# Performance work log

Hardware: AMD Instinct MI355X
Metric: run time of the kernel (lower is better)

## Reference

```python
import jax, jax.numpy as jnp
import numpy as np

NUM_BITS = 8
VMIN, VMAX = 0.0, 1.0
THRESH = 4.0
K_SYN = 32


def gray_code_encode(x):
    # (batch, features) -> (batch, features*NUM_BITS) binary float bits
    norm = (jnp.clip(x, VMIN, VMAX) - VMIN) / (VMAX - VMIN)
    levels = jnp.round(norm * (2 ** NUM_BITS - 1)).astype(jnp.int32)
    gray = levels ^ (levels >> 1)
    bit_pos = jnp.arange(NUM_BITS, dtype=jnp.int32)
    bits = ((gray[..., None] >> bit_pos) & 1).astype(jnp.float32)
    return bits.reshape(x.shape[0], -1)


def _make_sparse_weight(key, n_neurons, prev_size):
    # k random synapses per neuron with +/-1 weights (rest zero), as in
    # _initialise_layer_weights (standard, non-dynamic path)
    kc, ks = jax.random.split(key)
    cols = jax.random.randint(kc, (n_neurons, K_SYN), 0, prev_size)
    signs = jax.random.randint(ks, (n_neurons, K_SYN), 0, 2).astype(jnp.float32) * 2 - 1
    rows = jnp.broadcast_to(jnp.arange(n_neurons)[:, None], (n_neurons, K_SYN))
    return jnp.zeros((n_neurons, prev_size), jnp.float32).at[rows, cols].set(signs)


def setup_inputs() -> dict:
    key = jax.random.key(0)
    kx, k0, k1, k2, ko = jax.random.split(key, 5)
    batch, feat = 512, 256
    hidden, classes, n_hidden_layers = 4096, 1000, 3
    enc = feat * NUM_BITS  # 2048
    x = jax.random.uniform(kx, (batch, feat), dtype=jnp.float32)
    W0 = _make_sparse_weight(k0, hidden, enc)
    W1 = _make_sparse_weight(k1, hidden, hidden)
    W2 = _make_sparse_weight(k2, hidden, hidden)
    out_w = jax.random.normal(ko, (n_hidden_layers, hidden, classes), dtype=jnp.float32) * 0.01
    return {"x": x, "W0": W0, "W1": W1, "W2": W2, "out_w": out_w}


def reference(x, W0, W1, W2, out_w):
    prev = gray_code_encode(x)  # (b, enc)
    out = jnp.zeros((x.shape[0], out_w.shape[-1]), jnp.float32)
    for i, W in enumerate((W0, W1, W2)):
        z = prev @ W.T                                  # (b, hidden)
        prev = (z >= THRESH).astype(jnp.float32)        # binary activation
        out = out + prev @ out_w[i]                     # accumulate per-layer
    return out
```

## Files before the change

### kernel.cpp

```cpp
#include <hip/hip_runtime.h>
#include <stdint.h>

typedef unsigned long long u64;
typedef __attribute__((ext_vector_type(8))) short bf16x8;
typedef __attribute__((ext_vector_type(4))) float f32x4;
typedef __attribute__((ext_vector_type(4))) unsigned u32x4;

#define BATCH 512
#define FEAT 256
#define ENC 2048
#define HID 4096
#define CLS 1000
#define KTOT 12288
#define NSPLIT 16
#define KSPLIT 768
#define PARTLD 1024

#define OFF_ENC2   0
#define OFF_ACT2   131072
#define OFF_TABLE  917504
#define OFF_SGN    1703936
#define OFF_WT     2097152
#define OFF_PART   27262976
#define PART_BYTES (16ull * 512 * 1024 * 4)
#define WS_NEED    (OFF_PART + PART_BYTES)

static __device__ inline unsigned short f2bf(float f) {
    unsigned u = __float_as_uint(f);
    return (unsigned short)((u + 0x7FFFu + ((u >> 16) & 1u)) >> 16);
}

static __device__ inline void gld16(const void* g, void* s) {
    __builtin_amdgcn_global_load_lds((const __attribute__((address_space(1))) void*)g,
                                     (__attribute__((address_space(3))) void*)s, 16, 0, 0);
}

__global__ void __launch_bounds__(256)
k_prep(const float* __restrict__ x, u64* __restrict__ enc2,
       const float* __restrict__ W0, const float* __restrict__ W1,
       const float* __restrict__ W2,
       uint16_t* __restrict__ table, char* __restrict__ sgn,
       const float* __restrict__ out_w, short* __restrict__ wt) {
    __shared__ short tile[64 * 68];
    __shared__ int cnt4[4];
    int bid = blockIdx.x;
    int t = threadIdx.x;
    int lane = t & 63;
    int wv = t >> 6;

    if (bid < 512) {
        int wid = bid * 4 + wv;
        int f = wid >> 3, bg = wid & 7;
        float v = x[(size_t)(bg * 64 + lane) * FEAT + f];
        v = fminf(fmaxf(v, 0.0f), 1.0f);
        int lev = (int)rintf(v * 255.0f);
        unsigned gray = (unsigned)(lev ^ (lev >> 1));
        u64 w = 0;
        #pragma unroll
        for (int bit = 0; bit < 8; ++bit) {
            u64 m = __ballot((gray >> bit) & 1u);
            if (lane == bit) w = m;
        }
        if (lane < 8) enc2[(size_t)bg * ENC + f * 8 + lane] = w;
        return;
    }
    if (bid < 5632) {
        int wsid = (bid - 512) * 4 + wv;
        int row, base, cidx;
        if (wsid < HID) { row = wsid; base = 0; cidx = wv; }
        else {
            int w2 = wsid - HID;
            row = HID + (w2 >> 1);
            base = (w2 & 1) * 2048;
            cidx = wv >> 1;
        }
        uint16_t* te = table + (size_t)row * 32;
        char*     se = sgn + (size_t)row * 32;
        if (lane < 8) ((u64*)te)[lane] = 0;
        if (lane < 4) ((u64*)se)[lane] = 0;
        if (t < 4) cnt4[t] = 0;
        __syncthreads();
        const float* Wr;
        if (row < HID)          Wr = W0 + (size_t)row * ENC;
        else if (row < 2 * HID) Wr = W1 + (size_t)(row - HID) * HID + base;
        else                    Wr = W2 + (size_t)(row - 2 * HID) * HID + base;
        const u32x4* p4 = (const u32x4*)Wr;
        u32x4 v[8];
        #pragma unroll
        for (int j = 0; j < 8; ++j) v[j] = __builtin_nontemporal_load(p4 + j * 64 + lane);
        #pragma unroll
        for (int j = 0; j < 8; ++j) {
            unsigned a0 = v[j].x, a1 = v[j].y, a2 = v[j].z, a3 = v[j].w;
            if (a0 | a1 | a2 | a3) {
                int col0 = base + j * 256 + lane * 4;
                if (a0) { int s = atomicAdd(&cnt4[cidx], 1);
                          te[s] = (uint16_t)col0;       se[s] = (a0 >> 31) ? -1 : 1; }
                if (a1) { int s = atomicAdd(&cnt4[cidx], 1);
                          te[s] = (uint16_t)(col0 + 1); se[s] = (a1 >> 31) ? -1 : 1; }
                if (a2) { int s = atomicAdd(&cnt4[cidx], 1);
                          te[s] = (uint16_t)(col0 + 2); se[s] = (a2 >> 31) ? -1 : 1; }
                if (a3) { int s = atomicAdd(&cnt4[cidx], 1);
                          te[s] = (uint16_t)(col0 + 3); se[s] = (a3 >> 31) ? -1 : 1; }
            }
        }
        return;
    }
    {
        int b2 = bid - 5632;
        int kt = b2 % 192, ct = b2 / 192;
        int k0 = kt * 64, c0 = ct * 64;
        {
            int rrow = t >> 4, c4 = t & 15;
            int c = c0 + c4 * 4;
            #pragma unroll
            for (int rd = 0; rd < 4; ++rd) {
                int kl = rd * 16 + rrow;
                f32x4 vv;
                if (c < CLS)
                    vv = __builtin_nontemporal_load(
                        (const f32x4*)&out_w[(size_t)(k0 + kl) * CLS + c]);
                else { vv.x = 0.0f; vv.y = 0.0f; vv.z = 0.0f; vv.w = 0.0f; }
                short* d = &tile[kl * 68 + c4 * 4];
                d[0] = (short)f2bf(vv.x); d[1] = (short)f2bf(vv.y);
                d[2] = (short)f2bf(vv.z); d[3] = (short)f2bf(vv.w);
            }
        }
        __syncthreads();
        {
            int chunk = t & 7, cl2 = t >> 3;
            #pragma unroll
            for (int rd = 0; rd < 2; ++rd) {
                int c_local = rd * 32 + cl2;
                int c = c0 + c_local;
                unsigned s8[8];
                #pragma unroll
                for (int j = 0; j < 8; ++j)
                    s8[j] = (unsigned)(unsigned short)tile[(chunk * 8 + j) * 68 + c_local];
                uint4 pk;
                pk.x = s8[0] | (s8[1] << 16);
                pk.y = s8[2] | (s8[3] << 16);
                pk.z = s8[4] | (s8[5] << 16);
                pk.w = s8[6] | (s8[7] << 16);
                *(uint4*)&wt[(size_t)c * KTOT + k0 + ((chunk ^ (c & 7)) * 8)] = pk;
            }
        }
    }
}

__global__ void __launch_bounds__(256)
k_layer(const u64* __restrict__ prev2, int Kwords,
        const uint16_t* __restrict__ table_l, const char* __restrict__ sgn_l,
        u64* __restrict__ actout) {
    int wid = __builtin_amdgcn_readfirstlane(blockIdx.x * 4 + (threadIdx.x >> 6));
    int lane = threadIdx.x & 63;
    int n = wid >> 3, bg = wid & 7;
    const u64* prow = prev2 + (size_t)bg * Kwords;
    const uint4* tq = (const uint4*)(table_l + (size_t)n * 32);
    const int*  sq = (const int*)(sgn_l + (size_t)n * 32);
    int z = 0;
    #pragma unroll
    for (int q = 0; q < 4; ++q) {
        uint4 e4 = tq[q];
        int s0 = sq[q * 2], s1 = sq[q * 2 + 1];
        unsigned es[4] = {e4.x, e4.y, e4.z, e4.w};
        u64 w[8];
        #pragma unroll
        for (int h = 0; h < 4; ++h) {
            w[h * 2]     = prow[es[h] & 0xFFFFu];
            w[h * 2 + 1] = prow[es[h] >> 16];
        }
        #pragma unroll
        for (int j = 0; j < 8; ++j) {
            int bit = (int)((w[j] >> lane) & 1ull);
            int sw = (j < 4) ? s0 : s1;
            int s = (sw << (24 - (j & 3) * 8)) >> 24;
            z += s * bit;
        }
    }
    u64 res = __ballot(z >= 4);
    if (lane == 0) actout[(size_t)bg * HID + n] = res;
}

template<int MODE>
__global__ void __launch_bounds__(256)
k_gemm(const u64* __restrict__ act2, const short* __restrict__ wt,
       float* __restrict__ out, float* __restrict__ part) {
    __shared__ __attribute__((aligned(16))) short As[128 * 64];
    __shared__ __attribute__((aligned(16))) short Bs[128 * 64];
    int bid = blockIdx.x;
    int mt = bid & 3, nt = (bid >> 2) & 7, ks = bid >> 5;
    int tid = threadIdx.x, lane = tid & 63;
    int wv = tid >> 6, waveM = wv & 1, waveN = wv >> 1;
    int quad = lane >> 4, cl = lane & 15;
    f32x4 acc[4][4] = {};
    const char* Bb = (const char*)(wt + (size_t)nt * 128 * KTOT + ks * KSPLIT);
    int r = tid >> 3, sub = tid & 7;
    for (int kk = 0; kk < KSPLIT; kk += 64) {
        #pragma unroll
        for (int rd = 0; rd < 4; ++rd) {
            size_t go = (size_t)(r + rd * 32) * (KTOT * 2) + kk * 2 + sub * 16;
            gld16(Bb + go, &Bs[(tid + rd * 256) * 8]);
        }
        {
            int kabs = ks * KSPLIT + kk;
            int l = kabs >> 12, nk = kabs & 4095;
            #pragma unroll
            for (int i = 0; i < 4; ++i) {
                int item = i * 256 + tid;
                int rr = item >> 3, gg = item & 7;
                const u64* w8 = act2 + ((size_t)(l * 8 + mt * 2 + (rr >> 6))) * HID + nk + gg * 8;
                int bl = rr & 63;
                unsigned sh[8];
                #pragma unroll
                for (int j = 0; j < 8; ++j)
                    sh[j] = (unsigned)((w8[j] >> bl) & 1ull) * 0x3F80u;
                uint4 pk;
                pk.x = sh[0] | (sh[1] << 16);
                pk.y = sh[2] | (sh[3] << 16);
                pk.z = sh[4] | (sh[5] << 16);
                pk.w = sh[6] | (sh[7] << 16);
                *(uint4*)&As[rr * 64 + ((gg ^ (rr & 7)) * 8)] = pk;
            }
        }
        __syncthreads();
        #pragma unroll
        for (int s = 0; s < 2; ++s) {
            int xr = ((s * 4 + quad) ^ (cl & 7)) * 8;
            bf16x8 af[4], bfr[4];
            #pragma unroll
            for (int mf = 0; mf < 4; ++mf)
                af[mf] = *(const bf16x8*)&As[(waveM * 64 + mf * 16 + cl) * 64 + xr];
            #pragma unroll
            for (int nf = 0; nf < 4; ++nf)
                bfr[nf] = *(const bf16x8*)&Bs[(waveN * 64 + nf * 16 + cl) * 64 + xr];
            #pragma unroll
            for (int mf = 0; mf < 4; ++mf)
                #pragma unroll
                for (int nf = 0; nf < 4; ++nf)
                    acc[mf][nf] = __builtin_amdgcn_mfma_f32_16x16x32_bf16(
                        af[mf], bfr[nf], acc[mf][nf], 0, 0, 0);
        }
        __syncthreads();
    }
    if (MODE == 0) {
        float* pbase = part + (size_t)ks * (BATCH * PARTLD);
        #pragma unroll
        for (int mf = 0; mf < 4; ++mf)
            #pragma unroll
            for (int nf = 0; nf < 4; ++nf) {
                int cp = nt * 128 + waveN * 64 + nf * 16 + cl;
                #pragma unroll
                for (int rr = 0; rr < 4; ++rr) {
                    int mg = mt * 128 + waveM * 64 + mf * 16 + quad * 4 + rr;
                    pbase[(size_t)mg * PARTLD + cp] = acc[mf][nf][rr];
                }
            }
    } else {
        #pragma unroll
        for (int mf = 0; mf < 4; ++mf)
            #pragma unroll
            for (int nf = 0; nf < 4; ++nf) {
                int cp = nt * 128 + waveN * 64 + nf * 16 + cl;
                if (cp < CLS) {
                    #pragma unroll
                    for (int rr = 0; rr < 4; ++rr) {
                        int mg = mt * 128 + waveM * 64 + mf * 16 + quad * 4 + rr;
                        atomicAdd(&out[(size_t)mg * CLS + cp], acc[mf][nf][rr]);
                    }
                }
            }
    }
}

__global__ void k_reduce(const float* __restrict__ part, float* __restrict__ out) {
    int idx = blockIdx.x * blockDim.x + threadIdx.x;
    if (idx >= BATCH * (CLS / 4)) return;
    int b = idx / (CLS / 4), c4 = idx - b * (CLS / 4);
    f32x4 s = {0.f, 0.f, 0.f, 0.f};
    #pragma unroll
    for (int sp = 0; sp < NSPLIT; ++sp) {
        f32x4 v = *(const f32x4*)&part[((size_t)sp * BATCH + b) * PARTLD + c4 * 4];
        s.x += v.x; s.y += v.y; s.z += v.z; s.w += v.w;
    }
    *(f32x4*)&out[(size_t)b * CLS + c4 * 4] = s;
}

extern "C" void kernel_launch(void* const* d_in, const int* in_sizes, int n_in,
                              void* d_out, int out_size, void* d_ws, size_t ws_size,
                              hipStream_t stream) {
    const float* x     = (const float*)d_in[0];
    const float* W0    = (const float*)d_in[1];
    const float* W1    = (const float*)d_in[2];
    const float* W2    = (const float*)d_in[3];
    const float* out_w = (const float*)d_in[4];
    float* out = (float*)d_out;
    char* ws = (char*)d_ws;

    u64*      enc2   = (u64*)(ws + OFF_ENC2);
    u64*      act2   = (u64*)(ws + OFF_ACT2);
    uint16_t* table  = (uint16_t*)(ws + OFF_TABLE);
    char*     sgn    = (char*)(ws + OFF_SGN);
    short*    wt     = (short*)(ws + OFF_WT);
    float*    part   = (float*)(ws + OFF_PART);

    int use_part = (ws_size >= (size_t)WS_NEED) ? 1 : 0;

    hipLaunchKernelGGL(k_prep, dim3(8704), dim3(256), 0, stream,
                       x, enc2, W0, W1, W2, table, sgn, out_w, wt);
    if (!use_part)
        (void)hipMemsetAsync(d_out, 0, (size_t)BATCH * CLS * sizeof(float), stream);

    hipLaunchKernelGGL(k_layer, dim3(8192), dim3(256), 0, stream,
                       enc2, ENC, table, sgn, act2);
    hipLaunchKernelGGL(k_layer, dim3(8192), dim3(256), 0, stream,
                       act2, HID, table + (size_t)HID * 32, sgn + (size_t)HID * 32,
                       act2 + 8 * HID);
    hipLaunchKernelGGL(k_layer, dim3(8192), dim3(256), 0, stream,
                       act2 + 8 * HID, HID, table + (size_t)2 * HID * 32,
                       sgn + (size_t)2 * HID * 32, act2 + 16 * HID);
    if (use_part) {
        hipLaunchKernelGGL((k_gemm<0>), dim3(512), dim3(256), 0, stream,
                           act2, wt, out, part);
        hipLaunchKernelGGL(k_reduce, dim3((BATCH * (CLS / 4) + 255) / 256), dim3(256), 0,
                           stream, part, out);
    } else {
        hipLaunchKernelGGL((k_gemm<1>), dim3(512), dim3(256), 0, stream,
                           act2, wt, out, part);
    }
}
```

Before: 279.1 us.

## Compute sparse layer activations with bit-sliced carry-save adders per neuron lane

The sparse binary layer kernel now gives each lane one neuron and processes all 64 batch rows of a group as bits of a u64 word. It sums the 32 signed synapse bits with a bit-parallel carry-save adder tree and compares against a threshold using bitwise carry logic. The old version used one wavefront per neuron with per-lane bit extraction and a ballot. The prep kernel now packs sign and valid masks into two words per neuron instead of a per-synapse sign byte array. This cuts the layer grid from 8192 blocks of 256 threads to 512 blocks of 64 threads, which lowers occupancy and risks exposing the latency of the gather loads.

```diff
diff --git a/kernel.cpp b/kernel.cpp
--- a/kernel.cpp
+++ b/kernel.cpp
@@ -39,10 +39,11 @@
 k_prep(const float* __restrict__ x, u64* __restrict__ enc2,
        const float* __restrict__ W0, const float* __restrict__ W1,
        const float* __restrict__ W2,
-       uint16_t* __restrict__ table, char* __restrict__ sgn,
+       uint16_t* __restrict__ table, unsigned* __restrict__ bits,
        const float* __restrict__ out_w, short* __restrict__ wt) {
     __shared__ short tile[64 * 68];
     __shared__ int cnt4[4];
+    __shared__ int lneg[4];
     int bid = blockIdx.x;
     int t = threadIdx.x;
     int lane = t & 63;
@@ -75,10 +76,8 @@
             cidx = wv >> 1;
         }
         uint16_t* te = table + (size_t)row * 32;
-        char*     se = sgn + (size_t)row * 32;
         if (lane < 8) ((u64*)te)[lane] = 0;
-        if (lane < 4) ((u64*)se)[lane] = 0;
-        if (t < 4) cnt4[t] = 0;
+        if (t < 4) { cnt4[t] = 0; lneg[t] = 0; }
         __syncthreads();
         const float* Wr;
         if (row < HID)          Wr = W0 + (size_t)row * ENC;
@@ -93,15 +92,23 @@
             unsigned a0 = v[j].x, a1 = v[j].y, a2 = v[j].z, a3 = v[j].w;
             if (a0 | a1 | a2 | a3) {
                 int col0 = base + j * 256 + lane * 4;
-                if (a0) { int s = atomicAdd(&cnt4[cidx], 1);
-                          te[s] = (uint16_t)col0;       se[s] = (a0 >> 31) ? -1 : 1; }
-                if (a1) { int s = atomicAdd(&cnt4[cidx], 1);
-                          te[s] = (uint16_t)(col0 + 1); se[s] = (a1 >> 31) ? -1 : 1; }
-                if (a2) { int s = atomicAdd(&cnt4[cidx], 1);
-                          te[s] = (uint16_t)(col0 + 2); se[s] = (a2 >> 31) ? -1 : 1; }
-                if (a3) { int s = atomicAdd(&cnt4[cidx], 1);
-                          te[s] = (uint16_t)(col0 + 3); se[s] = (a3 >> 31) ? -1 : 1; }
-            }
+                if (a0) { int s = atomicAdd(&cnt4[cidx], 1); te[s] = (uint16_t)col0;
+                          if (a0 >> 31) atomicOr(&lneg[cidx], (int)(1u << s)); }
+                if (a1) { int s = atomicAdd(&cnt4[cidx], 1); te[s] = (uint16_t)(col0 + 1);
+                          if (a1 >> 31) atomicOr(&lneg[cidx], (int)(1u << s)); }
+                if (a2) { int s = atomicAdd(&cnt4[cidx], 1); te[s] = (uint16_t)(col0 + 2);
+                          if (a2 >> 31) atomicOr(&lneg[cidx], (int)(1u << s)); }
+                if (a3) { int s = atomicAdd(&cnt4[cidx], 1); te[s] = (uint16_t)(col0 + 3);
+                          if (a3 >> 31) atomicOr(&lneg[cidx], (int)(1u << s)); }
+            }
+        }
+        __syncthreads();
+        if (lane == 0) {
+            int cnt = cnt4[cidx];
+            unsigned nb = (unsigned)lneg[cidx];
+            unsigned vb = (cnt >= 32) ? 0xFFFFFFFFu : ((1u << cnt) - 1u);
+            uint2 pr; pr.x = nb; pr.y = vb;
+            *(uint2*)(bits + (size_t)row * 2) = pr;
         }
         return;
     }
@@ -147,38 +154,72 @@
     }
 }
 
-__global__ void __launch_bounds__(256)
+__global__ void __launch_bounds__(64)
 k_layer(const u64* __restrict__ prev2, int Kwords,
-        const uint16_t* __restrict__ table_l, const char* __restrict__ sgn_l,
+        const uint16_t* __restrict__ table_l, const unsigned* __restrict__ bits_l,
         u64* __restrict__ actout) {
-    int wid = __builtin_amdgcn_readfirstlane(blockIdx.x * 4 + (threadIdx.x >> 6));
-    int lane = threadIdx.x & 63;
-    int n = wid >> 3, bg = wid & 7;
+    int g = blockIdx.x >> 3, bg = blockIdx.x & 7;
+    int lane = threadIdx.x;
+    int n = (g << 6) + lane;
     const u64* prow = prev2 + (size_t)bg * Kwords;
     const uint4* tq = (const uint4*)(table_l + (size_t)n * 32);
-    const int*  sq = (const int*)(sgn_l + (size_t)n * 32);
-    int z = 0;
+    uint4 cw0 = tq[0], cw1 = tq[1], cw2 = tq[2], cw3 = tq[3];
+    uint2 bv = *(const uint2*)(bits_l + (size_t)n * 2);
+    unsigned negb = bv.x, valb = bv.y;
+
+    u64 P[4][4];
+    uint4 cwa[4] = {cw0, cw1, cw2, cw3};
     #pragma unroll
-    for (int q = 0; q < 4; ++q) {
-        uint4 e4 = tq[q];
-        int s0 = sq[q * 2], s1 = sq[q * 2 + 1];
-        unsigned es[4] = {e4.x, e4.y, e4.z, e4.w};
-        u64 w[8];
-        #pragma unroll
-        for (int h = 0; h < 4; ++h) {
-            w[h * 2]     = prow[es[h] & 0xFFFFu];
-            w[h * 2 + 1] = prow[es[h] >> 16];
-        }
-        #pragma unroll
-        for (int j = 0; j < 8; ++j) {
-            int bit = (int)((w[j] >> lane) & 1ull);
-            int sw = (j < 4) ? s0 : s1;
-            int s = (sw << (24 - (j & 3) * 8)) >> 24;
-            z += s * bit;
-        }
-    }
-    u64 res = __ballot(z >= 4);
-    if (lane == 0) actout[(size_t)bg * HID + n] = res;
+    for (int k = 0; k < 4; ++k) {
+        unsigned w0 = cwa[k].x, w1 = cwa[k].y, w2 = cwa[k].z, w3 = cwa[k].w;
+        unsigned cc[8] = { w0 & 0xFFFFu, w0 >> 16, w1 & 0xFFFFu, w1 >> 16,
+                           w2 & 0xFFFFu, w2 >> 16, w3 & 0xFFFFu, w3 >> 16 };
+        u64 u[8];
+        #pragma unroll
+        for (int e = 0; e < 8; ++e) {
+            int j = (k << 3) + e;
+            u64 w = prow[cc[e]];
+            u64 negm = 0ull - (u64)((negb >> j) & 1u);
+            u64 vm   = 0ull - (u64)((valb >> j) & 1u);
+            u[e] = (w ^ negm) & vm;
+        }
+        u64 s0, c0, s1, c1, s2, c2, b0, c3, t2, d0, b1, d1;
+        { u64 t = u[0] ^ u[1]; s0 = t ^ u[2]; c0 = (u[0] & u[1]) | (u[2] & t); }
+        { u64 t = u[3] ^ u[4]; s1 = t ^ u[5]; c1 = (u[3] & u[4]) | (u[5] & t); }
+        s2 = u[6] ^ u[7]; c2 = u[6] & u[7];
+        { u64 t = s0 ^ s1; b0 = t ^ s2; c3 = (s0 & s1) | (s2 & t); }
+        { u64 t = c0 ^ c1; t2 = t ^ c2; d0 = (c0 & c1) | (c2 & t); }
+        b1 = t2 ^ c3; d1 = t2 & c3;
+        P[k][0] = b0; P[k][1] = b1; P[k][2] = d0 ^ d1; P[k][3] = d0 & d1;
+    }
+    u64 A[5], B[5], U[6];
+    { u64 c;
+      { u64 t = P[0][0] ^ P[1][0]; A[0] = t; c = P[0][0] & P[1][0]; }
+      #pragma unroll
+      for (int i = 1; i < 4; ++i) {
+          u64 t = P[0][i] ^ P[1][i]; A[i] = t ^ c; c = (P[0][i] & P[1][i]) | (c & t); }
+      A[4] = c; }
+    { u64 c;
+      { u64 t = P[2][0] ^ P[3][0]; B[0] = t; c = P[2][0] & P[3][0]; }
+      #pragma unroll
+      for (int i = 1; i < 4; ++i) {
+          u64 t = P[2][i] ^ P[3][i]; B[i] = t ^ c; c = (P[2][i] & P[3][i]) | (c & t); }
+      B[4] = c; }
+    { u64 c;
+      { u64 t = A[0] ^ B[0]; U[0] = t; c = A[0] & B[0]; }
+      #pragma unroll
+      for (int i = 1; i < 5; ++i) {
+          u64 t = A[i] ^ B[i]; U[i] = t ^ c; c = (A[i] & B[i]) | (c & t); }
+      U[5] = c; }
+    int K = 60 - __popc(negb & valb);
+    u64 c = 0;
+    #pragma unroll
+    for (int i = 0; i < 6; ++i) {
+        u64 ki = 0ull - (u64)((K >> i) & 1);
+        u64 t = U[i] ^ ki;
+        c = (U[i] & ki) | (c & t);
+    }
+    actout[(size_t)bg * HID + n] = c;
 }
 
 template<int MODE>
@@ -299,25 +340,25 @@
     u64*      enc2   = (u64*)(ws + OFF_ENC2);
     u64*      act2   = (u64*)(ws + OFF_ACT2);
     uint16_t* table  = (uint16_t*)(ws + OFF_TABLE);
-    char*     sgn    = (char*)(ws + OFF_SGN);
+    unsigned* bits   = (unsigned*)(ws + OFF_SGN);
     short*    wt     = (short*)(ws + OFF_WT);
     float*    part   = (float*)(ws + OFF_PART);
 
     int use_part = (ws_size >= (size_t)WS_NEED) ? 1 : 0;
 
     hipLaunchKernelGGL(k_prep, dim3(8704), dim3(256), 0, stream,
-                       x, enc2, W0, W1, W2, table, sgn, out_w, wt);
+                       x, enc2, W0, W1, W2, table, bits, out_w, wt);
     if (!use_part)
         (void)hipMemsetAsync(d_out, 0, (size_t)BATCH * CLS * sizeof(float), stream);
 
-    hipLaunchKernelGGL(k_layer, dim3(8192), dim3(256), 0, stream,
-                       enc2, ENC, table, sgn, act2);
-    hipLaunchKernelGGL(k_layer, dim3(8192), dim3(256), 0, stream,
-                       act2, HID, table + (size_t)HID * 32, sgn + (size_t)HID * 32,
+    hipLaunchKernelGGL(k_layer, dim3(512), dim3(64), 0, stream,
+                       enc2, ENC, table, bits, act2);
+    hipLaunchKernelGGL(k_layer, dim3(512), dim3(64), 0, stream,
+                       act2, HID, table + (size_t)HID * 32, bits + (size_t)HID * 2,
                        act2 + 8 * HID);
-    hipLaunchKernelGGL(k_layer, dim3(8192), dim3(256), 0, stream,
+    hipLaunchKernelGGL(k_layer, dim3(512), dim3(64), 0, stream,
                        act2 + 8 * HID, HID, table + (size_t)2 * HID * 32,
-                       sgn + (size_t)2 * HID * 32, act2 + 16 * HID);
+                       bits + (size_t)2 * HID * 2, act2 + 16 * HID);
     if (use_part) {
         hipLaunchKernelGGL((k_gemm<0>), dim3(512), dim3(256), 0, stream,
                            act2, wt, out, part);
```

New measurement: 241.9 us. 13.3% less time.
